# Kernel optimization log

Measured on AMD Instinct MI355X. Metric: run time of the kernel, lower is better.

## Reference

```python
import jax, jax.numpy as jnp
import numpy as np

N_NODES = 50000
HEADS = 4
CH = 128
NEG_SLOPE = 0.2


def _gatv2_layer(x, src, dst, Wl, Wr, att, bias):
    # x: [N, Fin]; src/dst: [E'] (self-loops already appended)
    N = x.shape[0]
    xl = (x @ Wl).reshape(N, HEADS, CH)   # source-side transform
    xr = (x @ Wr).reshape(N, HEADS, CH)   # target-side transform
    e = jax.nn.leaky_relu(xl[src] + xr[dst], NEG_SLOPE)   # [E', H, C]
    logits = jnp.einsum('ehc,hc->eh', e, att)             # [E', H]
    # segment softmax over incoming edges of each destination node
    m = jax.ops.segment_max(logits, dst, num_segments=N)
    m = jnp.where(jnp.isfinite(m), m, 0.0)
    p = jnp.exp(logits - m[dst])
    denom = jax.ops.segment_sum(p, dst, num_segments=N)
    alpha = p / denom[dst]                                # [E', H]
    out = jax.ops.segment_sum(alpha[:, :, None] * xl[src], dst, num_segments=N)
    return out.reshape(N, HEADS * CH) + bias


def setup_inputs() -> dict:
    key = jax.random.key(0)
    ks = jax.random.split(key, 12)
    E = 400000
    x = jax.random.normal(ks[0], (N_NODES, 55), dtype=jnp.float32)
    edge_index = jax.random.randint(ks[1], (2, E), 0, N_NODES, dtype=jnp.int64)
    s = 0.1
    d1, d2 = 55, HEADS * CH
    return {
        'x': x,
        'edge_index': edge_index,
        'W1l': jax.random.normal(ks[2], (d1, d2), dtype=jnp.float32) * s,
        'W1r': jax.random.normal(ks[3], (d1, d2), dtype=jnp.float32) * s,
        'att1': jax.random.normal(ks[4], (HEADS, CH), dtype=jnp.float32) * s,
        'b1': jnp.zeros((d2,), dtype=jnp.float32),
        'W2l': jax.random.normal(ks[5], (d2, d2), dtype=jnp.float32) * s,
        'W2r': jax.random.normal(ks[6], (d2, d2), dtype=jnp.float32) * s,
        'att2': jax.random.normal(ks[7], (HEADS, CH), dtype=jnp.float32) * s,
        'b2': jnp.zeros((d2,), dtype=jnp.float32),
        'Wc': jax.random.normal(ks[8], (d2, 49), dtype=jnp.float32) * s,
        'bc': jnp.zeros((49,), dtype=jnp.float32),
    }


def reference(x, edge_index, W1l, W1r, att1, b1, W2l, W2r, att2, b2, Wc, bc):
    # add self loops once (PyG GATv2Conv default add_self_loops=True)
    loops = jnp.arange(N_NODES, dtype=edge_index.dtype)
    src = jnp.concatenate([edge_index[0], loops])
    dst = jnp.concatenate([edge_index[1], loops])
    h = _gatv2_layer(x, src, dst, W1l, W1r, att1, b1)
    h = jax.nn.elu(h)  # dropout is identity in eval mode
    h = _gatv2_layer(h, src, dst, W2l, W2r, att2, b2)
    h = jax.nn.elu(h)
    # forward applies conv2 a second time (conv3 unused in source)
    h = _gatv2_layer(h, src, dst, W2l, W2r, att2, b2)
    h = jax.nn.elu(h)
    return h @ Wc + bc
```

## Files before the change

### kernel.cpp

```cpp
#include <hip/hip_runtime.h>
#include <hip/hip_bf16.h>

constexpr int NN   = 50000;
constexpr int EE   = 400000;
constexpr int EP   = 450000;
constexpr int D    = 512;
constexpr int D2   = 1024;
constexpr int F0   = 55;
constexpr int F0P  = 64;
constexpr int OUTC = 49;

typedef __hip_bfloat16 bf16;

using frag_ab  = __attribute__((ext_vector_type(8))) short;
using frag_cd4 = __attribute__((ext_vector_type(4))) float;

__device__ inline void stf(float* p, float v) { *p = v; }
__device__ inline void stf(bf16* p, float v)  { *p = __float2bfloat16(v); }

__device__ inline void unpack8(uint4 u, float* f) {
    unsigned w[4] = {u.x, u.y, u.z, u.w};
    #pragma unroll
    for (int j = 0; j < 4; ++j) {
        __hip_bfloat162 h = *(__hip_bfloat162*)&w[j];
        float2 t = __bfloat1622float2(h);
        f[2 * j] = t.x; f[2 * j + 1] = t.y;
    }
}

template <typename TC, int NS>
__global__ __launch_bounds__(512) void gemm_8p(
    const bf16* __restrict__ A,
    const bf16* __restrict__ Bt,
    TC* __restrict__ C,
    const float* __restrict__ bias,
    int M, int Ncs)
{
    constexpr int K  = NS * 64;
    constexpr int BM = 256, BN = 128, BK = 64;
    __shared__ __align__(16) bf16 As[3][BM * BK];
    __shared__ __align__(16) bf16 Bs[3][BN * BK];

    int bx = blockIdx.x, by = blockIdx.y;
    if (gridDim.x == 8) {
        int bid = by * 8 + bx;
        bx = (bid >> 3) & 7;
        by = (bid & 7) + ((bid >> 6) << 3);
    }
    if (by * BM >= M) return;

    const int tid = threadIdx.x;
    const int w   = tid >> 6;
    const int l   = tid & 63;
    const int rowBase = by * BM;
    const int colBase = bx * BN;

    const bf16* gA[4];
    #pragma unroll
    for (int j = 0; j < 4; ++j) {
        int c = j * 512 + tid;
        int row = c >> 3, chs = (c & 7) ^ (row & 7);
        int ar = rowBase + row; if (ar >= M) ar = M - 1;
        gA[j] = A + (size_t)ar * K + chs * 8;
    }
    const bf16* gB[2];
    #pragma unroll
    for (int j = 0; j < 2; ++j) {
        int c = j * 512 + tid;
        int row = c >> 3, chs = (c & 7) ^ (row & 7);
        gB[j] = Bt + (size_t)(colBase + row) * K + chs * 8;
    }

    const int l15 = l & 15, l4 = l >> 4;
    const int wm = (w >> 1) * 64;
    const int wn = (w & 1) * 64;
    int aoff[4][2], boff[4][2];
    #pragma unroll
    for (int i = 0; i < 4; ++i) {
        int ra = wm + i * 16 + l15;
        int rb = wn + i * 16 + l15;
        #pragma unroll
        for (int ks = 0; ks < 2; ++ks) {
            aoff[i][ks] = ra * BK + (((ks * 4 + l4) ^ (ra & 7)) * 8);
            boff[i][ks] = rb * BK + (((ks * 4 + l4) ^ (rb & 7)) * 8);
        }
    }

    frag_cd4 acc[4][4] = {};

    auto stage = [&](int s, int p) {
        int slot = s % 3;
        if (p < 4) {
            bf16* dst = &As[slot][(p * 512 + w * 64) * 8];
            __builtin_amdgcn_global_load_lds(
                (const __attribute__((address_space(1))) void*)(gA[p] + s * BK),
                (__attribute__((address_space(3))) void*)dst, 16, 0, 0);
        } else {
            int j = p - 4;
            bf16* dst = &Bs[slot][(j * 512 + w * 64) * 8];
            __builtin_amdgcn_global_load_lds(
                (const __attribute__((address_space(1))) void*)(gB[j] + s * BK),
                (__attribute__((address_space(3))) void*)dst, 16, 0, 0);
        }
    };

    #pragma unroll
    for (int p = 0; p < 6; ++p) stage(0, p);
    if (NS > 1) {
        #pragma unroll
        for (int p = 0; p < 6; ++p) stage(1, p);
    }

    #pragma unroll
    for (int s = 0; s < NS; ++s) {
        if (s + 1 < NS) asm volatile("s_waitcnt vmcnt(6)" ::: "memory");
        else            asm volatile("s_waitcnt vmcnt(0)" ::: "memory");
        __builtin_amdgcn_s_barrier();
        asm volatile("" ::: "memory");

        const bf16* Ab = As[s % 3];
        const bf16* Bb = Bs[s % 3];

        frag_ab bfr[4][2];
        #pragma unroll
        for (int ni = 0; ni < 4; ++ni)
            #pragma unroll
            for (int ks = 0; ks < 2; ++ks)
                bfr[ni][ks] = *(const frag_ab*)&Bb[boff[ni][ks]];
        frag_ab afr[2][2];
        #pragma unroll
        for (int mi = 0; mi < 2; ++mi)
            #pragma unroll
            for (int ks = 0; ks < 2; ++ks)
                afr[mi][ks] = *(const frag_ab*)&Ab[aoff[mi][ks]];
        if (s + 2 < NS) { stage(s + 2, 0); stage(s + 2, 1); stage(s + 2, 2); }

        __builtin_amdgcn_s_barrier();
        asm volatile("" ::: "memory");
        __builtin_amdgcn_s_setprio(1);
        #pragma unroll
        for (int mi = 0; mi < 2; ++mi)
            #pragma unroll
            for (int ni = 0; ni < 4; ++ni)
                #pragma unroll
                for (int ks = 0; ks < 2; ++ks)
                    acc[mi][ni] = __builtin_amdgcn_mfma_f32_16x16x32_bf16(
                        afr[mi][ks], bfr[ni][ks], acc[mi][ni], 0, 0, 0);
        __builtin_amdgcn_s_setprio(0);
        __builtin_amdgcn_s_barrier();
        asm volatile("" ::: "memory");

        frag_ab afr2[2][2];
        #pragma unroll
        for (int mi = 0; mi < 2; ++mi)
            #pragma unroll
            for (int ks = 0; ks < 2; ++ks)
                afr2[mi][ks] = *(const frag_ab*)&Ab[aoff[mi + 2][ks]];
        if (s + 2 < NS) { stage(s + 2, 3); stage(s + 2, 4); stage(s + 2, 5); }

        __builtin_amdgcn_s_barrier();
        asm volatile("" ::: "memory");
        __builtin_amdgcn_s_setprio(1);
        #pragma unroll
        for (int mi = 0; mi < 2; ++mi)
            #pragma unroll
            for (int ni = 0; ni < 4; ++ni)
                #pragma unroll
                for (int ks = 0; ks < 2; ++ks)
                    acc[mi + 2][ni] = __builtin_amdgcn_mfma_f32_16x16x32_bf16(
                        afr2[mi][ks], bfr[ni][ks], acc[mi + 2][ni], 0, 0, 0);
        __builtin_amdgcn_s_setprio(0);
    }

    #pragma unroll
    for (int mi = 0; mi < 4; ++mi) {
        #pragma unroll
        for (int r = 0; r < 4; ++r) {
            int row = rowBase + wm + mi * 16 + l4 * 4 + r;
            if (row >= M) continue;
            #pragma unroll
            for (int ni = 0; ni < 4; ++ni) {
                int col = colBase + wn + ni * 16 + l15;
                if (col >= Ncs) continue;
                float v = acc[mi][ni][r];
                if (bias) v += bias[col];
                stf(&C[(size_t)row * Ncs + col], v);
            }
        }
    }
}

__global__ void convert_transpose2(const float* __restrict__ W0,
                                   const float* __restrict__ W1,
                                   bf16* __restrict__ Wt) {
    __shared__ float tile[32][33];
    const float* W = blockIdx.z ? W1 : W0;
    bf16* dst = Wt + (size_t)blockIdx.z * D * D;
    int bn = blockIdx.x * 32, bk = blockIdx.y * 32;
    int tx = threadIdx.x & 31, ty = threadIdx.x >> 5;
    #pragma unroll
    for (int i = 0; i < 32; i += 8)
        tile[ty + i][tx] = W[(size_t)(bk + ty + i) * D + bn + tx];
    __syncthreads();
    #pragma unroll
    for (int i = 0; i < 32; i += 8)
        dst[(size_t)(bn + ty + i) * D + bk + tx] = __float2bfloat16(tile[tx][ty + i]);
}

__global__ void pad_convert_x(const float* __restrict__ x, bf16* __restrict__ Xp) {
    int idx = blockIdx.x * blockDim.x + threadIdx.x;
    if (idx >= NN * F0P) return;
    int n = idx >> 6, t = idx & 63;
    float v = (t < F0) ? x[n * F0 + t] : 0.f;
    Xp[idx] = __float2bfloat16(v);
}

__global__ void conv_transpose_w1(const float* __restrict__ Wl,
                                  const float* __restrict__ Wr,
                                  bf16* __restrict__ Wt) {
    const float* W = blockIdx.y ? Wr : Wl;
    bf16* dst = Wt + (size_t)blockIdx.y * D * F0P;
    int n = blockIdx.x;
    int k = threadIdx.x;
    float v = (k < F0) ? W[(size_t)k * D + n] : 0.f;
    dst[n * F0P + k] = __float2bfloat16(v);
}

__global__ void conv_transpose_wc(const float* __restrict__ W, bf16* __restrict__ Wt) {
    int n = blockIdx.x;
    for (int k = threadIdx.x; k < D; k += blockDim.x) {
        float v = (n < OUTC) ? W[(size_t)k * OUTC + n] : 0.f;
        Wt[(size_t)n * D + k] = __float2bfloat16(v);
    }
}

__global__ void zero_ints(int* __restrict__ p, int n) {
    int i = blockIdx.x * blockDim.x + threadIdx.x;
    if (i < n) p[i] = 0;
}

__global__ void count_dst(const int* __restrict__ dstIdx, int* __restrict__ cnt) {
    int e = blockIdx.x * blockDim.x + threadIdx.x;
    if (e >= EP) return;
    int dst = (e < EE) ? dstIdx[e] : (e - EE);
    atomicAdd(&cnt[dst], 1);
}

__global__ void scan_blocks(const int* __restrict__ cnt, int* __restrict__ off,
                            int* __restrict__ bsum) {
    __shared__ int sh[1024];
    int i = blockIdx.x * 1024 + threadIdx.x;
    int v = (i < NN) ? cnt[i] : 0;
    sh[threadIdx.x] = v;
    __syncthreads();
    #pragma unroll
    for (int d = 1; d < 1024; d <<= 1) {
        int t = (threadIdx.x >= d) ? sh[threadIdx.x - d] : 0;
        __syncthreads();
        sh[threadIdx.x] += t;
        __syncthreads();
    }
    if (i < NN) off[i] = sh[threadIdx.x] - v;
    if (threadIdx.x == 1023) bsum[blockIdx.x] = sh[1023];
}

__global__ void scan_bsums(int* __restrict__ bsum, int* __restrict__ bbase,
                           int* __restrict__ off, int nb) {
    int lane = threadIdx.x;
    int orig = (lane < nb) ? bsum[lane] : 0;
    int v = orig;
    #pragma unroll
    for (int d = 1; d < 64; d <<= 1) {
        int t = __shfl_up(v, d);
        if (lane >= d) v += t;
    }
    if (lane < nb) bbase[lane] = v - orig;
    if (lane == 63) off[NN] = v;
}

__global__ void add_base(int* __restrict__ off, const int* __restrict__ bbase) {
    int i = blockIdx.x * 1024 + threadIdx.x;
    if (blockIdx.x == 0 || i >= NN) return;
    off[i] += bbase[blockIdx.x];
}

__global__ void fill_srcpos(const int* __restrict__ srcIdx, const int* __restrict__ dstIdx,
                            const int* __restrict__ off, int* __restrict__ cnt,
                            int* __restrict__ srcPos) {
    int e = blockIdx.x * blockDim.x + threadIdx.x;
    if (e >= EP) return;
    int dst = (e < EE) ? dstIdx[e] : (e - EE);
    int src = (e < EE) ? srcIdx[e] : (e - EE);
    int pos = off[dst] + atomicAdd(&cnt[dst], 1);
    srcPos[pos] = src;
}

__global__ __launch_bounds__(256) void gat_edge_fused(
    const bf16* __restrict__ XLR, const float* __restrict__ att,
    const int* __restrict__ off, const int* __restrict__ srcPos,
    const float* __restrict__ bias, bf16* __restrict__ Hout)
{
    int v = blockIdx.x * 4 + (threadIdx.x >> 6);
    if (v >= NN) return;
    int lane = threadIdx.x & 63;

    uint4 ru = *(const uint4*)(XLR + (size_t)v * D2 + D + lane * 8);
    float xr[8]; unpack8(ru, xr);
    const float4* a4 = (const float4*)(att + lane * 8);
    float4 aa = a4[0], ab = a4[1];
    float at[8] = {aa.x, aa.y, aa.z, aa.w, ab.x, ab.y, ab.z, ab.w};

    int s0 = off[v], s1 = off[v + 1];
    float den = 0.f;
    float acc[8] = {};

    uint4 lb0 = {0, 0, 0, 0}, lb1 = {0, 0, 0, 0};
    if (s0 < s1)     lb0 = *(const uint4*)(XLR + (size_t)srcPos[s0] * D2 + lane * 8);
    if (s0 + 1 < s1) lb1 = *(const uint4*)(XLR + (size_t)srcPos[s0 + 1] * D2 + lane * 8);

    for (int i = s0; i < s1; ++i) {
        uint4 cur = lb0;
        lb0 = lb1;
        if (i + 2 < s1)
            lb1 = *(const uint4*)(XLR + (size_t)srcPos[i + 2] * D2 + lane * 8);

        float xl[8]; unpack8(cur, xl);
        float sa = 0.f, sb = 0.f;
        #pragma unroll
        for (int j = 0; j < 4; ++j) {
            float t = xl[j] + xr[j];
            t = fmaxf(t, 0.2f * t);
            sa = fmaf(t, at[j], sa);
        }
        #pragma unroll
        for (int j = 4; j < 8; ++j) {
            float t = xl[j] + xr[j];
            t = fmaxf(t, 0.2f * t);
            sb = fmaf(t, at[j], sb);
        }
        float s = sa + sb;
        s += __shfl_xor(s, 1);
        s += __shfl_xor(s, 2);
        s += __shfl_xor(s, 4);
        s += __shfl_xor(s, 8);
        s = fminf(fmaxf(s, -60.f), 60.f);
        float p = __expf(s);
        den += p;
        #pragma unroll
        for (int j = 0; j < 8; ++j) acc[j] = fmaf(p, xl[j], acc[j]);
    }
    float r = 1.f / den;

    const float4* b4 = (const float4*)(bias + lane * 8);
    float4 ba = b4[0], bb = b4[1];
    float bi[8] = {ba.x, ba.y, ba.z, ba.w, bb.x, bb.y, bb.z, bb.w};
    uint4 ou;
    unsigned* ow = (unsigned*)&ou;
    #pragma unroll
    for (int j = 0; j < 4; ++j) {
        float o0 = acc[2 * j] * r + bi[2 * j];
        float o1 = acc[2 * j + 1] * r + bi[2 * j + 1];
        o0 = o0 > 0.f ? o0 : (__expf(o0) - 1.f);
        o1 = o1 > 0.f ? o1 : (__expf(o1) - 1.f);
        __hip_bfloat162 h{__float2bfloat16(o0), __float2bfloat16(o1)};
        ow[j] = *(unsigned*)&h;
    }
    *(uint4*)(Hout + (size_t)v * D + lane * 8) = ou;
}

extern "C" void kernel_launch(void* const* d_in, const int* in_sizes, int n_in,
                              void* d_out, int out_size, void* d_ws, size_t ws_size,
                              hipStream_t stream) {
    const float* x    = (const float*)d_in[0];
    const int*   ei   = (const int*)d_in[1];
    const float* W1l  = (const float*)d_in[2];
    const float* W1r  = (const float*)d_in[3];
    const float* att1 = (const float*)d_in[4];
    const float* b1   = (const float*)d_in[5];
    const float* W2l  = (const float*)d_in[6];
    const float* W2r  = (const float*)d_in[7];
    const float* att2 = (const float*)d_in[8];
    const float* b2   = (const float*)d_in[9];
    const float* Wc   = (const float*)d_in[10];
    const float* bc   = (const float*)d_in[11];
    float* out = (float*)d_out;

    const int* srcIdx = ei;
    const int* dstIdx = ei + EE;

    constexpr int NB = (NN + 1023) / 1024;

    bf16* XLR  = (bf16*)d_ws;
    bf16* Hb   = XLR + (size_t)NN * D2;
    bf16* Xpad = Hb + (size_t)NN * D;
    bf16* W2T  = Xpad + (size_t)NN * F0P;
    bf16* W1T  = W2T + (size_t)D2 * D;
    bf16* WcT  = W1T + (size_t)D2 * F0P;
    int* cnt   = (int*)(WcT + (size_t)128 * D);
    int* cnt2  = cnt + NN;
    int* off   = cnt2 + NN;
    int* srcPos= off + (NN + 1);
    int* bsum  = srcPos + EP;
    int* bbase = bsum + NB;

    zero_ints<<<(2 * NN + 255) / 256, 256, 0, stream>>>(cnt, 2 * NN);
    count_dst<<<(EP + 255) / 256, 256, 0, stream>>>(dstIdx, cnt);
    scan_blocks<<<NB, 1024, 0, stream>>>(cnt, off, bsum);
    scan_bsums<<<1, 64, 0, stream>>>(bsum, bbase, off, NB);
    add_base<<<NB, 1024, 0, stream>>>(off, bbase);
    fill_srcpos<<<(EP + 255) / 256, 256, 0, stream>>>(srcIdx, dstIdx, off, cnt2, srcPos);

    dim3 ctGrid(D / 32, D / 32, 2);
    convert_transpose2<<<ctGrid, 256, 0, stream>>>(W2l, W2r, W2T);
    dim3 w1Grid(D, 2);
    conv_transpose_w1<<<w1Grid, F0P, 0, stream>>>(W1l, W1r, W1T);
    conv_transpose_wc<<<128, 256, 0, stream>>>(Wc, WcT);
    pad_convert_x<<<(NN * F0P + 255) / 256, 256, 0, stream>>>(x, Xpad);

    int gy = (((NN + 255) / 256) + 7) / 8 * 8 + 8;
    dim3 gemmGrid(D2 / 128, gy);
    int nodeBlocks = (NN + 3) / 4;

    gemm_8p<bf16, 1><<<gemmGrid, 512, 0, stream>>>(Xpad, W1T, XLR, nullptr, NN, D2);
    gat_edge_fused<<<nodeBlocks, 256, 0, stream>>>(XLR, att1, off, srcPos, b1, Hb);

    for (int rep = 0; rep < 2; ++rep) {
        gemm_8p<bf16, 8><<<gemmGrid, 512, 0, stream>>>(Hb, W2T, XLR, nullptr, NN, D2);
        gat_edge_fused<<<nodeBlocks, 256, 0, stream>>>(XLR, att2, off, srcPos, b2, Hb);
    }

    dim3 gridc(1, (NN + 255) / 256);
    gemm_8p<float, 8><<<gridc, 512, 0, stream>>>(Hb, WcT, out, bc, NN, OUTC);
}
```

Baseline: 606.3 us.

## Halve GEMM K-tile to shrink LDS and single-phase the main loop

The GEMM now uses a K-tile of 32 instead of 64, which halves shared memory per block, and declares launch bounds targeting more resident blocks per CU. The main loop drops from two half-phases with four barriers to one barrier per stage, with the prefetch issued right after it. The swizzle is adapted to the narrower rows, and the grid drops its extra row of padding blocks. The aim is higher occupancy and less sync overhead, at the cost of twice as many K iterations and less compute per barrier.

```diff
diff --git a/kernel.cpp b/kernel.cpp
--- a/kernel.cpp
+++ b/kernel.cpp
@@ -29,15 +29,15 @@
 }
 
 template <typename TC, int NS>
-__global__ __launch_bounds__(512) void gemm_8p(
+__global__ __launch_bounds__(512, 4) void gemm_dp(
     const bf16* __restrict__ A,
     const bf16* __restrict__ Bt,
     TC* __restrict__ C,
     const float* __restrict__ bias,
     int M, int Ncs)
 {
-    constexpr int K  = NS * 64;
-    constexpr int BM = 256, BN = 128, BK = 64;
+    constexpr int K  = NS * 32;
+    constexpr int BM = 256, BN = 128, BK = 32;
     __shared__ __align__(16) bf16 As[3][BM * BK];
     __shared__ __align__(16) bf16 Bs[3][BN * BK];
 
@@ -55,120 +55,78 @@
     const int rowBase = by * BM;
     const int colBase = bx * BN;
 
-    const bf16* gA[4];
-    #pragma unroll
-    for (int j = 0; j < 4; ++j) {
-        int c = j * 512 + tid;
-        int row = c >> 3, chs = (c & 7) ^ (row & 7);
+    const bf16* gA[2];
+    #pragma unroll
+    for (int j = 0; j < 2; ++j) {
+        int f = j * 512 + tid;
+        int row = f >> 2, c = (f & 3) ^ ((row >> 1) & 3);
         int ar = rowBase + row; if (ar >= M) ar = M - 1;
-        gA[j] = A + (size_t)ar * K + chs * 8;
-    }
-    const bf16* gB[2];
-    #pragma unroll
-    for (int j = 0; j < 2; ++j) {
-        int c = j * 512 + tid;
-        int row = c >> 3, chs = (c & 7) ^ (row & 7);
-        gB[j] = Bt + (size_t)(colBase + row) * K + chs * 8;
+        gA[j] = A + (size_t)ar * K + c * 8;
+    }
+    const bf16* gB;
+    {
+        int f = tid;
+        int row = f >> 2, c = (f & 3) ^ ((row >> 1) & 3);
+        gB = Bt + (size_t)(colBase + row) * K + c * 8;
     }
 
     const int l15 = l & 15, l4 = l >> 4;
     const int wm = (w >> 1) * 64;
     const int wn = (w & 1) * 64;
-    int aoff[4][2], boff[4][2];
+    int aoff[4], boff[4];
     #pragma unroll
     for (int i = 0; i < 4; ++i) {
         int ra = wm + i * 16 + l15;
         int rb = wn + i * 16 + l15;
-        #pragma unroll
-        for (int ks = 0; ks < 2; ++ks) {
-            aoff[i][ks] = ra * BK + (((ks * 4 + l4) ^ (ra & 7)) * 8);
-            boff[i][ks] = rb * BK + (((ks * 4 + l4) ^ (rb & 7)) * 8);
-        }
+        aoff[i] = ra * BK + ((l4 ^ ((ra >> 1) & 3)) * 8);
+        boff[i] = rb * BK + ((l4 ^ ((rb >> 1) & 3)) * 8);
     }
 
     frag_cd4 acc[4][4] = {};
 
-    auto stage = [&](int s, int p) {
+    auto stage = [&](int s) {
         int slot = s % 3;
-        if (p < 4) {
-            bf16* dst = &As[slot][(p * 512 + w * 64) * 8];
-            __builtin_amdgcn_global_load_lds(
-                (const __attribute__((address_space(1))) void*)(gA[p] + s * BK),
-                (__attribute__((address_space(3))) void*)dst, 16, 0, 0);
-        } else {
-            int j = p - 4;
-            bf16* dst = &Bs[slot][(j * 512 + w * 64) * 8];
-            __builtin_amdgcn_global_load_lds(
-                (const __attribute__((address_space(1))) void*)(gB[j] + s * BK),
-                (__attribute__((address_space(3))) void*)dst, 16, 0, 0);
-        }
+        __builtin_amdgcn_global_load_lds(
+            (const __attribute__((address_space(1))) void*)(gA[0] + s * BK),
+            (__attribute__((address_space(3))) void*)(&As[slot][(w * 64) * 8]),
+            16, 0, 0);
+        __builtin_amdgcn_global_load_lds(
+            (const __attribute__((address_space(1))) void*)(gA[1] + s * BK),
+            (__attribute__((address_space(3))) void*)(&As[slot][(512 + w * 64) * 8]),
+            16, 0, 0);
+        __builtin_amdgcn_global_load_lds(
+            (const __attribute__((address_space(1))) void*)(gB + s * BK),
+            (__attribute__((address_space(3))) void*)(&Bs[slot][(w * 64) * 8]),
+            16, 0, 0);
     };
 
-    #pragma unroll
-    for (int p = 0; p < 6; ++p) stage(0, p);
-    if (NS > 1) {
-        #pragma unroll
-        for (int p = 0; p < 6; ++p) stage(1, p);
-    }
+    stage(0);
+    if (NS > 1) stage(1);
 
     #pragma unroll
     for (int s = 0; s < NS; ++s) {
-        if (s + 1 < NS) asm volatile("s_waitcnt vmcnt(6)" ::: "memory");
+        if (s + 1 < NS) asm volatile("s_waitcnt vmcnt(3)" ::: "memory");
         else            asm volatile("s_waitcnt vmcnt(0)" ::: "memory");
         __builtin_amdgcn_s_barrier();
         asm volatile("" ::: "memory");
 
+        if (s + 2 < NS) stage(s + 2);
+
         const bf16* Ab = As[s % 3];
         const bf16* Bb = Bs[s % 3];
-
-        frag_ab bfr[4][2];
-        #pragma unroll
-        for (int ni = 0; ni < 4; ++ni)
+        frag_ab a[4], b[4];
+        #pragma unroll
+        for (int i = 0; i < 4; ++i) a[i] = *(const frag_ab*)&Ab[aoff[i]];
+        #pragma unroll
+        for (int n = 0; n < 4; ++n) b[n] = *(const frag_ab*)&Bb[boff[n]];
+
+        __builtin_amdgcn_s_setprio(1);
+        #pragma unroll
+        for (int i = 0; i < 4; ++i)
             #pragma unroll
-            for (int ks = 0; ks < 2; ++ks)
-                bfr[ni][ks] = *(const frag_ab*)&Bb[boff[ni][ks]];
-        frag_ab afr[2][2];
-        #pragma unroll
-        for (int mi = 0; mi < 2; ++mi)
-            #pragma unroll
-            for (int ks = 0; ks < 2; ++ks)
-                afr[mi][ks] = *(const frag_ab*)&Ab[aoff[mi][ks]];
-        if (s + 2 < NS) { stage(s + 2, 0); stage(s + 2, 1); stage(s + 2, 2); }
-
-        __builtin_amdgcn_s_barrier();
-        asm volatile("" ::: "memory");
-        __builtin_amdgcn_s_setprio(1);
-        #pragma unroll
-        for (int mi = 0; mi < 2; ++mi)
-            #pragma unroll
-            for (int ni = 0; ni < 4; ++ni)
-                #pragma unroll
-                for (int ks = 0; ks < 2; ++ks)
-                    acc[mi][ni] = __builtin_amdgcn_mfma_f32_16x16x32_bf16(
-                        afr[mi][ks], bfr[ni][ks], acc[mi][ni], 0, 0, 0);
-        __builtin_amdgcn_s_setprio(0);
-        __builtin_amdgcn_s_barrier();
-        asm volatile("" ::: "memory");
-
-        frag_ab afr2[2][2];
-        #pragma unroll
-        for (int mi = 0; mi < 2; ++mi)
-            #pragma unroll
-            for (int ks = 0; ks < 2; ++ks)
-                afr2[mi][ks] = *(const frag_ab*)&Ab[aoff[mi + 2][ks]];
-        if (s + 2 < NS) { stage(s + 2, 3); stage(s + 2, 4); stage(s + 2, 5); }
-
-        __builtin_amdgcn_s_barrier();
-        asm volatile("" ::: "memory");
-        __builtin_amdgcn_s_setprio(1);
-        #pragma unroll
-        for (int mi = 0; mi < 2; ++mi)
-            #pragma unroll
-            for (int ni = 0; ni < 4; ++ni)
-                #pragma unroll
-                for (int ks = 0; ks < 2; ++ks)
-                    acc[mi + 2][ni] = __builtin_amdgcn_mfma_f32_16x16x32_bf16(
-                        afr2[mi][ks], bfr[ni][ks], acc[mi + 2][ni], 0, 0, 0);
+            for (int n = 0; n < 4; ++n)
+                acc[i][n] = __builtin_amdgcn_mfma_f32_16x16x32_bf16(
+                    a[i], b[n], acc[i][n], 0, 0, 0);
         __builtin_amdgcn_s_setprio(0);
     }
 
@@ -417,18 +375,19 @@
     conv_transpose_wc<<<128, 256, 0, stream>>>(Wc, WcT);
     pad_convert_x<<<(NN * F0P + 255) / 256, 256, 0, stream>>>(x, Xpad);
 
-    int gy = (((NN + 255) / 256) + 7) / 8 * 8 + 8;
+    int panels = (NN + 255) / 256;
+    int gy = (panels + 7) / 8 * 8;
     dim3 gemmGrid(D2 / 128, gy);
     int nodeBlocks = (NN + 3) / 4;
 
-    gemm_8p<bf16, 1><<<gemmGrid, 512, 0, stream>>>(Xpad, W1T, XLR, nullptr, NN, D2);
+    gemm_dp<bf16, 2><<<gemmGrid, 512, 0, stream>>>(Xpad, W1T, XLR, nullptr, NN, D2);
     gat_edge_fused<<<nodeBlocks, 256, 0, stream>>>(XLR, att1, off, srcPos, b1, Hb);
 
     for (int rep = 0; rep < 2; ++rep) {
-        gemm_8p<bf16, 8><<<gemmGrid, 512, 0, stream>>>(Hb, W2T, XLR, nullptr, NN, D2);
+        gemm_dp<bf16, 16><<<gemmGrid, 512, 0, stream>>>(Hb, W2T, XLR, nullptr, NN, D2);
         gat_edge_fused<<<nodeBlocks, 256, 0, stream>>>(XLR, att2, off, srcPos, b2, Hb);
     }
 
-    dim3 gridc(1, (NN + 255) / 256);
-    gemm_8p<float, 8><<<gridc, 512, 0, stream>>>(Hb, WcT, out, bc, NN, OUTC);
-}
+    dim3 gridc(1, panels);
+    gemm_dp<float, 16><<<gridc, 512, 0, stream>>>(Hb, WcT, out, bc, NN, OUTC);
+}
```

Result: faster. 565.9 us (median of 2 runs) (-6.7%).
